# Kernel tuning notes

Measured on AMD Instinct MI355X. Metric: run time of the kernel, lower is better.

The kernel has to match this reference:

```python
import jax, jax.numpy as jnp
import numpy as np

NEG = -9e15

def _gat_layer(x, adj, W, a_src, a_dst):
    # x: [B,N,Fin], W: [Fin,Fout], a_src/a_dst: [Fout], adj: [N,N]
    h = jnp.einsum('bnf,fo->bno', x, W)                    # [B,N,Fout]
    e_src = jnp.einsum('bno,o->bn', h, a_src)              # [B,N]
    e_dst = jnp.einsum('bno,o->bn', h, a_dst)              # [B,N]
    e = jax.nn.leaky_relu(e_src[:, :, None] + e_dst[:, None, :], 0.2)  # [B,N,N]
    att = jax.nn.softmax(jnp.where(adj > 0, e, NEG), axis=-1)
    return jnp.einsum('bij,bjo->bio', att, h)              # [B,N,Fout]

def setup_inputs() -> dict:
    key = jax.random.key(0)
    ks = jax.random.split(key, 12)
    B, N, Fin = 8, 2048, 128
    H = [128, 128, 64]
    C = 128
    s = lambda *d: 1.0 / np.sqrt(d[0])
    inp = {
        'x':   jax.random.normal(ks[0], (B, N, Fin), jnp.float32),
        'adj': jax.random.normal(ks[1], (N, N), jnp.float32),
        'W1':  jax.random.normal(ks[2], (Fin, H[0]), jnp.float32) * s(Fin),
        'a1s': jax.random.normal(ks[3], (H[0],), jnp.float32) * s(H[0]),
        'a1d': jax.random.normal(ks[4], (H[0],), jnp.float32) * s(H[0]),
        'W2':  jax.random.normal(ks[5], (H[0], H[1]), jnp.float32) * s(H[0]),
        'a2s': jax.random.normal(ks[6], (H[1],), jnp.float32) * s(H[1]),
        'a2d': jax.random.normal(ks[7], (H[1],), jnp.float32) * s(H[1]),
        'W3':  jax.random.normal(ks[8], (H[1], H[2]), jnp.float32) * s(H[1]),
        'a3s': jax.random.normal(ks[9], (H[2],), jnp.float32) * s(H[2]),
        'a3d': jax.random.normal(ks[10], (H[2],), jnp.float32) * s(H[2]),
        'Wlin': jax.random.normal(ks[11], (H[2] * N, C), jnp.float32) * s(H[2] * N),
        'blin': jnp.zeros((C,), jnp.float32),
    }
    return inp

def reference(x, adj, W1, a1s, a1d, W2, a2s, a2d, W3, a3s, a3d, Wlin, blin):
    out = jax.nn.relu(_gat_layer(x, adj, W1, a1s, a1d))
    out = jax.nn.relu(_gat_layer(out, adj, W2, a2s, a2d))
    out = jax.nn.relu(_gat_layer(out, adj, W3, a3s, a3d))
    B = out.shape[0]
    out = out.reshape(B, -1)              # flatten [B, N*H3]
    return out @ Wlin + blin              # [B, num_classes]
```

## Files before the change

### kernel.cpp

```cpp
#include <hip/hip_runtime.h>
#include <stdint.h>


typedef unsigned short u16;
typedef __bf16 bf16x8 __attribute__((ext_vector_type(8)));
typedef float f32x4 __attribute__((ext_vector_type(4)));
typedef u16 u16x8 __attribute__((ext_vector_type(8)));

#define LOG2E 1.44269504088896340736f

__device__ __forceinline__ float b2f(u16 u) {
    union { unsigned int i; float f; } v; v.i = ((unsigned int)u) << 16; return v.f;
}
__device__ __forceinline__ u16 f2b(float f) {
    union { float f; unsigned int i; } v; v.f = f;
    unsigned int i = v.i;
    return (u16)((i + 0x7fffu + ((i >> 16) & 1u)) >> 16);
}
__device__ __forceinline__ float fast_exp2(float x) {
#if __has_builtin(__builtin_amdgcn_exp2f)
    return __builtin_amdgcn_exp2f(x);
#else
    return exp2f(x);
#endif
}

union ABfrag { bf16x8 v; u16x8 u; };

__device__ __forceinline__ void gload_lds16(const u16* g, u16* l) {
    __builtin_amdgcn_global_load_lds((const __attribute__((address_space(1))) void*)g,
                                     (__attribute__((address_space(3))) void*)l,
                                     16, 0, 0);
}

__global__ void __launch_bounds__(256) k_mask(const float* __restrict__ adj,
                                              uint32_t* __restrict__ adjm) {
    const int w = threadIdx.x >> 6, lane = threadIdx.x & 63;
    const int row = blockIdx.x * 4 + w;
    const float* ar = adj + (size_t)row * 2048;
    uint32_t* mr = adjm + (size_t)row * 64;
    for (int j0 = 0; j0 < 2048; j0 += 64) {
        unsigned long long m = __ballot(ar[j0 + lane] > 0.f);
        if (lane == 0) {
            mr[(j0 >> 5)] = (uint32_t)m;
            mr[(j0 >> 5) + 1] = (uint32_t)(m >> 32);
        }
    }
}

__global__ void k_prep(const float* __restrict__ W1, const float* __restrict__ W2,
                       const float* __restrict__ W3,
                       const float* __restrict__ a1s, const float* __restrict__ a1d,
                       const float* __restrict__ a2s, const float* __restrict__ a2d,
                       const float* __restrict__ a3s, const float* __restrict__ a3d,
                       u16* __restrict__ Wt1, u16* __restrict__ Wt2, u16* __restrict__ Wt3,
                       float* __restrict__ u1s, float* __restrict__ u1d,
                       float* __restrict__ u2s, float* __restrict__ u2d,
                       float* __restrict__ u3s, float* __restrict__ u3d) {
    if (blockIdx.x == 160) {
        int f = threadIdx.x;
        if (f < 128) {
            float s1 = 0.f, d1 = 0.f, s2 = 0.f, d2 = 0.f, s3 = 0.f, d3 = 0.f;
            for (int o = 0; o < 128; ++o) { float w = W1[f * 128 + o]; s1 += w * a1s[o]; d1 += w * a1d[o]; }
            for (int o = 0; o < 128; ++o) { float w = W2[f * 128 + o]; s2 += w * a2s[o]; d2 += w * a2d[o]; }
            for (int o = 0; o <  64; ++o) { float w = W3[f *  64 + o]; s3 += w * a3s[o]; d3 += w * a3d[o]; }
            u1s[f] = s1 * LOG2E; u1d[f] = d1 * LOG2E;
            u2s[f] = s2 * LOG2E; u2d[f] = d2 * LOG2E;
            u3s[f] = s3 * LOG2E; u3d[f] = d3 * LOG2E;
        }
        return;
    }
    int idx = blockIdx.x * 256 + threadIdx.x;
    if (idx < 16384) {
        int f = idx >> 7, o = idx & 127;
        Wt1[o * 128 + f] = f2b(W1[idx]);
    } else if (idx < 32768) {
        int j = idx - 16384; int f = j >> 7, o = j & 127;
        Wt2[o * 128 + f] = f2b(W2[j]);
    } else if (idx < 40960) {
        int j = idx - 32768; int f = j >> 6, o = j & 63;
        Wt3[o * 128 + f] = f2b(W3[j]);
    }
}

template <int F, bool XF32>
__global__ void __launch_bounds__(256) k_h(const void* __restrict__ xv,
                                           const u16* __restrict__ Wt,
                                           const float* __restrict__ us,
                                           const float* __restrict__ ud,
                                           u16* __restrict__ h_t,
                                           float* __restrict__ es2,
                                           float* __restrict__ ed2) {
    constexpr int NT = F / 16;
    constexpr int TNP = 72;
    __shared__ __align__(16) u16 hl[F * TNP];

    const int b = blockIdx.x;
    const int nblk = blockIdx.y;
    const int tid = threadIdx.x;
    const int w = tid >> 6, lane = tid & 63;
    const int quad = lane >> 4, l15 = lane & 15;
    const int n0w = nblk * 64 + w * 16;
    const int i_a = n0w + l15;

    ABfrag afr[4];
    float ps = 0.f, pd = 0.f;
    if (XF32) {
        const float* xr = (const float*)xv + ((size_t)(b * 2048 + i_a)) * 128;
#pragma unroll
        for (int kk = 0; kk < 4; ++kk) {
            const int o8 = kk * 32 + quad * 8;
            float4 x0 = *reinterpret_cast<const float4*>(xr + o8);
            float4 x1 = *reinterpret_cast<const float4*>(xr + o8 + 4);
            float4 s0 = *reinterpret_cast<const float4*>(us + o8);
            float4 s1 = *reinterpret_cast<const float4*>(us + o8 + 4);
            float4 d0 = *reinterpret_cast<const float4*>(ud + o8);
            float4 d1 = *reinterpret_cast<const float4*>(ud + o8 + 4);
            ps += x0.x * s0.x + x0.y * s0.y + x0.z * s0.z + x0.w * s0.w
                + x1.x * s1.x + x1.y * s1.y + x1.z * s1.z + x1.w * s1.w;
            pd += x0.x * d0.x + x0.y * d0.y + x0.z * d0.z + x0.w * d0.w
                + x1.x * d1.x + x1.y * d1.y + x1.z * d1.z + x1.w * d1.w;
            afr[kk].u[0] = f2b(x0.x); afr[kk].u[1] = f2b(x0.y);
            afr[kk].u[2] = f2b(x0.z); afr[kk].u[3] = f2b(x0.w);
            afr[kk].u[4] = f2b(x1.x); afr[kk].u[5] = f2b(x1.y);
            afr[kk].u[6] = f2b(x1.z); afr[kk].u[7] = f2b(x1.w);
        }
    } else {
        const u16* xr = (const u16*)xv + ((size_t)(b * 2048 + i_a)) * 128;
#pragma unroll
        for (int kk = 0; kk < 4; ++kk) {
            const int o8 = kk * 32 + quad * 8;
            u16x8 xa = *reinterpret_cast<const u16x8*>(xr + o8);
            afr[kk].u = xa;
            float4 s0 = *reinterpret_cast<const float4*>(us + o8);
            float4 s1 = *reinterpret_cast<const float4*>(us + o8 + 4);
            float4 d0 = *reinterpret_cast<const float4*>(ud + o8);
            float4 d1 = *reinterpret_cast<const float4*>(ud + o8 + 4);
            float xf[8];
#pragma unroll
            for (int j = 0; j < 8; ++j) xf[j] = b2f(xa[j]);
            ps += xf[0] * s0.x + xf[1] * s0.y + xf[2] * s0.z + xf[3] * s0.w
                + xf[4] * s1.x + xf[5] * s1.y + xf[6] * s1.z + xf[7] * s1.w;
            pd += xf[0] * d0.x + xf[1] * d0.y + xf[2] * d0.z + xf[3] * d0.w
                + xf[4] * d1.x + xf[5] * d1.y + xf[6] * d1.z + xf[7] * d1.w;
        }
    }
    ps += __shfl_xor(ps, 16, 64); ps += __shfl_xor(ps, 32, 64);
    pd += __shfl_xor(pd, 16, 64); pd += __shfl_xor(pd, 32, 64);
    if (quad == 0) {
        es2[b * 2048 + i_a] = ps;
        ed2[b * 2048 + i_a] = pd;
    }

    f32x4 acc[NT];
#pragma unroll
    for (int nt = 0; nt < NT; ++nt) acc[nt] = (f32x4){0.f, 0.f, 0.f, 0.f};
#pragma unroll
    for (int kk = 0; kk < 4; ++kk) {
#pragma unroll
        for (int nt = 0; nt < NT; ++nt) {
            bf16x8 bfv = *reinterpret_cast<const bf16x8*>(
                Wt + (nt * 16 + l15) * 128 + kk * 32 + quad * 8);
            acc[nt] = __builtin_amdgcn_mfma_f32_16x16x32_bf16(afr[kk].v, bfv, acc[nt], 0, 0, 0);
        }
    }

#pragma unroll
    for (int nt = 0; nt < NT; ++nt)
#pragma unroll
        for (int r = 0; r < 4; ++r)
            hl[(nt * 16 + l15) * TNP + w * 16 + quad * 4 + r] = f2b(acc[nt][r]);
    __syncthreads();
    if (tid < F * 2) {
        int o = tid >> 1, half = tid & 1;
        const u16* src = hl + o * TNP + half * 32;
        u16* dst = h_t + ((size_t)(b * F + o)) * 2048 + nblk * 64 + half * 32;
#pragma unroll
        for (int c = 0; c < 4; ++c)
            *reinterpret_cast<u16x8*>(dst + c * 8) =
                *reinterpret_cast<const u16x8*>(src + c * 8);
    }
}

template <int F, bool OUT_F32>
__global__ void __launch_bounds__(512) k_attn(const float* __restrict__ es2,
                                              const float* __restrict__ ed2,
                                              const uint32_t* __restrict__ adjm,
                                              const u16* __restrict__ h_t,
                                              void* __restrict__ outp) {
    constexpr int NT = F / 16;
    __shared__ __align__(16) u16 Ht[2][2][F * 64];
    __shared__ float dLDS[2][64];
    float* accLDS = (float*)&Ht[0][0][0];

    const int b = blockIdx.x;
    const int iblk = blockIdx.y;
    const int tid = threadIdx.x;
    const int grp = tid >> 8;
    const int t8 = tid & 255;
    const int w = t8 >> 6;
    const int lane = tid & 63;
    const int quad = lane >> 4, l15 = lane & 15;
    const int i_a = iblk * 64 + w * 16 + l15;

    const float esv = es2[b * 2048 + i_a];
    const float* edb = ed2 + b * 2048;
    const uint2* mrow = (const uint2*)(adjm + (size_t)i_a * 64);
    const u16* hb = h_t + (size_t)b * F * 2048;

    const int lro = lane >> 3;
    const int lcp = lane & 7;
    const int jt0 = grp * 16;

    f32x4 acc[NT];
#pragma unroll
    for (int nt = 0; nt < NT; ++nt) acc[nt] = (f32x4){0.f, 0.f, 0.f, 0.f};
    float dacc = 0.f;

    {
        const int j0 = jt0 * 64;
#pragma unroll
        for (int it = 0; it < F / 32; ++it) {
            int ro = (it * 4 + w) * 8 + lro;
            int c = lcp ^ (ro & 7);
            gload_lds16(hb + (size_t)ro * 2048 + j0 + c * 8, &Ht[grp][0][(it * 4 + w) * 512]);
        }
    }
    float4 ec0 = *reinterpret_cast<const float4*>(edb + jt0 * 64 + quad * 8);
    float4 ec1 = *reinterpret_cast<const float4*>(edb + jt0 * 64 + quad * 8 + 4);
    float4 ec2 = *reinterpret_cast<const float4*>(edb + jt0 * 64 + quad * 8 + 32);
    float4 ec3 = *reinterpret_cast<const float4*>(edb + jt0 * 64 + quad * 8 + 36);
    uint2 mc = mrow[jt0];
    __syncthreads();

    for (int jj = 0; jj < 16; ++jj) {
        const int cur = jj & 1, nxt = cur ^ 1;
        float4 en0, en1, en2, en3; uint2 mn;
        if (jj < 15) {
            const int j1 = (jt0 + jj + 1) * 64;
#pragma unroll
            for (int it = 0; it < F / 32; ++it) {
                int ro = (it * 4 + w) * 8 + lro;
                int c = lcp ^ (ro & 7);
                gload_lds16(hb + (size_t)ro * 2048 + j1 + c * 8, &Ht[grp][nxt][(it * 4 + w) * 512]);
            }
            en0 = *reinterpret_cast<const float4*>(edb + j1 + quad * 8);
            en1 = *reinterpret_cast<const float4*>(edb + j1 + quad * 8 + 4);
            en2 = *reinterpret_cast<const float4*>(edb + j1 + quad * 8 + 32);
            en3 = *reinterpret_cast<const float4*>(edb + j1 + quad * 8 + 36);
            mn = mrow[jt0 + jj + 1];
        }

        ABfrag af[2];
        {
            float ed[16] = {ec0.x, ec0.y, ec0.z, ec0.w, ec1.x, ec1.y, ec1.z, ec1.w,
                            ec2.x, ec2.y, ec2.z, ec2.w, ec3.x, ec3.y, ec3.z, ec3.w};
#pragma unroll
            for (int kk = 0; kk < 2; ++kk) {
                uint32_t word = kk ? mc.y : mc.x;
#pragma unroll
                for (int jx = 0; jx < 8; ++jx) {
                    float e = esv + ed[kk * 8 + jx];
                    float v = fmaxf(e, 0.2f * e);
                    float wv = fast_exp2(v);
                    bool bit = (word >> (quad * 8 + jx)) & 1u;
                    wv = bit ? wv : 0.f;
                    u16 wb = f2b(wv);
                    af[kk].u[jx] = wb;
                    dacc += b2f(wb);
                }
            }
        }

#pragma unroll
        for (int kk = 0; kk < 2; ++kk) {
#pragma unroll
            for (int nt = 0; nt < NT; ++nt) {
                int ob = nt * 16 + l15;
                int c = kk * 4 + quad;
                bf16x8 bfv = *reinterpret_cast<const bf16x8*>(
                    &Ht[grp][cur][ob * 64 + ((c ^ (ob & 7)) * 8)]);
                acc[nt] = __builtin_amdgcn_mfma_f32_16x16x32_bf16(af[kk].v, bfv, acc[nt], 0, 0, 0);
            }
        }

        if (jj < 15) { ec0 = en0; ec1 = en1; ec2 = en2; ec3 = en3; mc = mn; }
        __syncthreads();
    }

    dacc += __shfl_xor(dacc, 16, 64);
    dacc += __shfl_xor(dacc, 32, 64);
    if (quad == 0) dLDS[grp][w * 16 + l15] = dacc;
    if (grp == 1) {
#pragma unroll
        for (int nt = 0; nt < NT; ++nt)
            *reinterpret_cast<f32x4*>(&accLDS[(t8 * NT + nt) * 4]) = acc[nt];
    }
    __syncthreads();
    if (grp == 0) {
#pragma unroll
        for (int nt = 0; nt < NT; ++nt)
            acc[nt] += *reinterpret_cast<const f32x4*>(&accLDS[(t8 * NT + nt) * 4]);
        float dinv[4];
#pragma unroll
        for (int r = 0; r < 4; ++r) {
            int row = w * 16 + quad * 4 + r;
            dinv[r] = 1.0f / fmaxf(dLDS[0][row] + dLDS[1][row], 1e-30f);
        }
        const int ib = iblk * 64 + w * 16 + quad * 4;
        if (OUT_F32) {
            float* o3 = (float*)outp;
#pragma unroll
            for (int nt = 0; nt < NT; ++nt)
#pragma unroll
                for (int r = 0; r < 4; ++r) {
                    float vv = fmaxf(acc[nt][r] * dinv[r], 0.f);
                    o3[((size_t)(b * 2048 + ib + r)) * F + nt * 16 + l15] = vv;
                }
        } else {
            u16* xo = (u16*)outp;
#pragma unroll
            for (int nt = 0; nt < NT; ++nt)
#pragma unroll
                for (int r = 0; r < 4; ++r) {
                    float vv = fmaxf(acc[nt][r] * dinv[r], 0.f);
                    xo[((size_t)(b * 2048 + ib + r)) * F + nt * 16 + l15] = f2b(vv);
                }
        }
    }
}

__global__ void __launch_bounds__(256) k_lin(const float* __restrict__ o3,
                                             const float* __restrict__ Wlin,
                                             float* __restrict__ pbuf) {
    __shared__ float xc[8][256];
    __shared__ float red[8][8][128];
    const int tid = threadIdx.x;
    const int k0 = blockIdx.x * 256;
    for (int idx = tid; idx < 2048; idx += 256) {
        int bb = idx >> 8, kk = idx & 255;
        xc[bb][kk] = o3[(size_t)bb * 131072 + k0 + kk];
    }
    __syncthreads();
    const int o4 = tid & 31;
    const int kb = tid >> 5;
    f32x4 acc[8];
#pragma unroll
    for (int bb = 0; bb < 8; ++bb) acc[bb] = (f32x4){0.f, 0.f, 0.f, 0.f};
    const float* wp = Wlin + (size_t)(k0 + kb * 32) * 128 + o4 * 4;
#pragma unroll 4
    for (int k = 0; k < 32; ++k) {
        f32x4 wv = *reinterpret_cast<const f32x4*>(wp + (size_t)k * 128);
#pragma unroll
        for (int bb = 0; bb < 8; ++bb) acc[bb] += wv * xc[bb][kb * 32 + k];
    }
#pragma unroll
    for (int bb = 0; bb < 8; ++bb)
        *reinterpret_cast<f32x4*>(&red[kb][bb][o4 * 4]) = acc[bb];
    __syncthreads();
    const int f = tid * 4;
    const int bb = f >> 7, o = f & 127;
    f32x4 s = (f32x4){0.f, 0.f, 0.f, 0.f};
#pragma unroll
    for (int k2 = 0; k2 < 8; ++k2) s += *reinterpret_cast<const f32x4*>(&red[k2][bb][o]);
    *reinterpret_cast<f32x4*>(&pbuf[(size_t)blockIdx.x * 1024 + f]) = s;
}

__global__ void __launch_bounds__(256) k_bias(const float* __restrict__ pbuf,
                                              const float* __restrict__ blin,
                                              float* __restrict__ out) {
    __shared__ float red[256];
    const int tid = threadIdx.x;
    const int p16 = tid >> 4;
    const int fo = tid & 15;
    const int f0 = blockIdx.x * 16;
    float s = 0.f;
#pragma unroll 4
    for (int p = p16; p < 512; p += 16)
        s += pbuf[(size_t)p * 1024 + f0 + fo];
    red[tid] = s;
    __syncthreads();
    if (tid < 16) {
        float t = 0.f;
#pragma unroll
        for (int k = 0; k < 16; ++k) t += red[k * 16 + tid];
        out[f0 + tid] = t + blin[(f0 + tid) & 127];
    }
}

extern "C" void kernel_launch(void* const* d_in, const int* in_sizes, int n_in,
                              void* d_out, int out_size, void* d_ws, size_t ws_size,
                              hipStream_t stream) {
    (void)in_sizes; (void)n_in; (void)out_size;
    const float* x    = (const float*)d_in[0];
    const float* adj  = (const float*)d_in[1];
    const float* W1   = (const float*)d_in[2];
    const float* a1s  = (const float*)d_in[3];
    const float* a1d  = (const float*)d_in[4];
    const float* W2   = (const float*)d_in[5];
    const float* a2s  = (const float*)d_in[6];
    const float* a2d  = (const float*)d_in[7];
    const float* W3   = (const float*)d_in[8];
    const float* a3s  = (const float*)d_in[9];
    const float* a3d  = (const float*)d_in[10];
    const float* Wlin = (const float*)d_in[11];
    const float* blin = (const float*)d_in[12];

    char* ws = (char*)d_ws;
    u16*   h_t = (u16*)ws;
    size_t off = (size_t)4 << 20;
    float* es2 = (float*)(ws + off); off += 65536;
    float* ed2 = (float*)(ws + off); off += 65536;
    u16*   Wt1 = (u16*)(ws + off);   off += 32768;
    u16*   Wt2 = (u16*)(ws + off);   off += 32768;
    u16*   Wt3 = (u16*)(ws + off);   off += 16384;
    float* u1s = (float*)(ws + off); off += 512;
    float* u1d = (float*)(ws + off); off += 512;
    float* u2s = (float*)(ws + off); off += 512;
    float* u2d = (float*)(ws + off); off += 512;
    float* u3s = (float*)(ws + off); off += 512;
    float* u3d = (float*)(ws + off); off += 512;
    uint32_t* adjm = (uint32_t*)(ws + off); off += 524288;
    float* pbuf = (float*)(ws + off); off += (size_t)512 * 1024 * 4;
    u16* actA;
    if (ws_size >= off + ((size_t)4 << 20)) {
        actA = (u16*)(ws + off);
    } else {
        actA = (u16*)d_in[0];
    }
    float* o3 = (float*)actA;

    dim3 g(8, 32);
    k_mask<<<512, 256, 0, stream>>>(adj, adjm);
    k_prep<<<161, 256, 0, stream>>>(W1, W2, W3, a1s, a1d, a2s, a2d, a3s, a3d,
                                    Wt1, Wt2, Wt3, u1s, u1d, u2s, u2d, u3s, u3d);

    k_h<128, true ><<<g, 256, 0, stream>>>((const void*)x, Wt1, u1s, u1d, h_t, es2, ed2);
    k_attn<128, false><<<g, 512, 0, stream>>>(es2, ed2, adjm, h_t, (void*)actA);

    k_h<128, false><<<g, 256, 0, stream>>>((const void*)actA, Wt2, u2s, u2d, h_t, es2, ed2);
    k_attn<128, false><<<g, 512, 0, stream>>>(es2, ed2, adjm, h_t, (void*)actA);

    k_h<64, false><<<g, 256, 0, stream>>>((const void*)actA, Wt3, u3s, u3d, h_t, es2, ed2);
    k_attn<64, true ><<<g, 512, 0, stream>>>(es2, ed2, adjm, h_t, (void*)o3);

    k_lin<<<512, 256, 0, stream>>>(o3, Wlin, pbuf);
    k_bias<<<64, 256, 0, stream>>>(pbuf, blin, (float*)d_out);
}
```

Before: 260.1 us.

## Factor exp of leaky-relu logits into per-node exponentials and MFMA row sums

Precomputes exp2 of source and destination scores (and of their 0.2-scaled versions) per node in the projection kernel. The attention kernel then forms each weight as the max of two products, with no per-edge exp. The softmax denominator is accumulated by an extra MFMA against a ones fragment instead of scalar adds and shuffles. This removes per-edge transcendental and VALU work, at the cost of doubled score storage and a possible overflow or precision change from the product form.

Result: no change. 264.6 us (+1.7%).

```diff
diff --git a/kernel.cpp b/kernel.cpp
--- a/kernel.cpp
+++ b/kernel.cpp
@@ -89,8 +89,8 @@
                                            const float* __restrict__ us,
                                            const float* __restrict__ ud,
                                            u16* __restrict__ h_t,
-                                           float* __restrict__ es2,
-                                           float* __restrict__ ed2) {
+                                           float* __restrict__ esf,
+                                           float* __restrict__ edf) {
     constexpr int NT = F / 16;
     constexpr int TNP = 72;
     __shared__ __align__(16) u16 hl[F * TNP];
@@ -148,8 +148,11 @@
     ps += __shfl_xor(ps, 16, 64); ps += __shfl_xor(ps, 32, 64);
     pd += __shfl_xor(pd, 16, 64); pd += __shfl_xor(pd, 32, 64);
     if (quad == 0) {
-        es2[b * 2048 + i_a] = ps;
-        ed2[b * 2048 + i_a] = pd;
+        const size_t idx = (size_t)(b * 2048 + i_a) * 2;
+        float2 sv; sv.x = fast_exp2(ps); sv.y = fast_exp2(0.2f * ps);
+        float2 dv; dv.x = fast_exp2(pd); dv.y = fast_exp2(0.2f * pd);
+        *reinterpret_cast<float2*>(esf + idx) = sv;
+        *reinterpret_cast<float2*>(edf + idx) = dv;
     }
 
     f32x4 acc[NT];
@@ -183,14 +186,13 @@
 }
 
 template <int F, bool OUT_F32>
-__global__ void __launch_bounds__(512) k_attn(const float* __restrict__ es2,
-                                              const float* __restrict__ ed2,
+__global__ void __launch_bounds__(512) k_attn(const float* __restrict__ esf,
+                                              const float* __restrict__ edf,
                                               const uint32_t* __restrict__ adjm,
                                               const u16* __restrict__ h_t,
                                               void* __restrict__ outp) {
     constexpr int NT = F / 16;
     __shared__ __align__(16) u16 Ht[2][2][F * 64];
-    __shared__ float dLDS[2][64];
     float* accLDS = (float*)&Ht[0][0][0];
 
     const int b = blockIdx.x;
@@ -203,8 +205,9 @@
     const int quad = lane >> 4, l15 = lane & 15;
     const int i_a = iblk * 64 + w * 16 + l15;
 
-    const float esv = es2[b * 2048 + i_a];
-    const float* edb = ed2 + b * 2048;
+    const float2 esp = *reinterpret_cast<const float2*>(esf + ((size_t)(b * 2048 + i_a)) * 2);
+    const float Es = esp.x, Fs = esp.y;
+    const float* edb = edf + (size_t)b * 4096;
     const uint2* mrow = (const uint2*)(adjm + (size_t)i_a * 64);
     const u16* hb = h_t + (size_t)b * F * 2048;
 
@@ -212,10 +215,14 @@
     const int lcp = lane & 7;
     const int jt0 = grp * 16;
 
+    ABfrag onesf;
+#pragma unroll
+    for (int j = 0; j < 8; ++j) onesf.u[j] = 0x3F80;
+
     f32x4 acc[NT];
 #pragma unroll
     for (int nt = 0; nt < NT; ++nt) acc[nt] = (f32x4){0.f, 0.f, 0.f, 0.f};
-    float dacc = 0.f;
+    f32x4 dccc = (f32x4){0.f, 0.f, 0.f, 0.f};
 
     {
         const int j0 = jt0 * 64;
@@ -226,16 +233,21 @@
             gload_lds16(hb + (size_t)ro * 2048 + j0 + c * 8, &Ht[grp][0][(it * 4 + w) * 512]);
         }
     }
-    float4 ec0 = *reinterpret_cast<const float4*>(edb + jt0 * 64 + quad * 8);
-    float4 ec1 = *reinterpret_cast<const float4*>(edb + jt0 * 64 + quad * 8 + 4);
-    float4 ec2 = *reinterpret_cast<const float4*>(edb + jt0 * 64 + quad * 8 + 32);
-    float4 ec3 = *reinterpret_cast<const float4*>(edb + jt0 * 64 + quad * 8 + 36);
+    f32x4 ec[8];
+    {
+        const float* eb = edb + (size_t)(jt0 * 64 + quad * 8) * 2;
+#pragma unroll
+        for (int q = 0; q < 4; ++q) ec[q] = *reinterpret_cast<const f32x4*>(eb + q * 4);
+#pragma unroll
+        for (int q = 0; q < 4; ++q) ec[4 + q] = *reinterpret_cast<const f32x4*>(eb + 64 + q * 4);
+    }
     uint2 mc = mrow[jt0];
     __syncthreads();
 
+#pragma unroll 2
     for (int jj = 0; jj < 16; ++jj) {
         const int cur = jj & 1, nxt = cur ^ 1;
-        float4 en0, en1, en2, en3; uint2 mn;
+        f32x4 en[8]; uint2 mn;
         if (jj < 15) {
             const int j1 = (jt0 + jj + 1) * 64;
 #pragma unroll
@@ -244,31 +256,29 @@
                 int c = lcp ^ (ro & 7);
                 gload_lds16(hb + (size_t)ro * 2048 + j1 + c * 8, &Ht[grp][nxt][(it * 4 + w) * 512]);
             }
-            en0 = *reinterpret_cast<const float4*>(edb + j1 + quad * 8);
-            en1 = *reinterpret_cast<const float4*>(edb + j1 + quad * 8 + 4);
-            en2 = *reinterpret_cast<const float4*>(edb + j1 + quad * 8 + 32);
-            en3 = *reinterpret_cast<const float4*>(edb + j1 + quad * 8 + 36);
+            const float* eb = edb + (size_t)(j1 + quad * 8) * 2;
+#pragma unroll
+            for (int q = 0; q < 4; ++q) en[q] = *reinterpret_cast<const f32x4*>(eb + q * 4);
+#pragma unroll
+            for (int q = 0; q < 4; ++q) en[4 + q] = *reinterpret_cast<const f32x4*>(eb + 64 + q * 4);
             mn = mrow[jt0 + jj + 1];
         }
 
         ABfrag af[2];
-        {
-            float ed[16] = {ec0.x, ec0.y, ec0.z, ec0.w, ec1.x, ec1.y, ec1.z, ec1.w,
-                            ec2.x, ec2.y, ec2.z, ec2.w, ec3.x, ec3.y, ec3.z, ec3.w};
-#pragma unroll
-            for (int kk = 0; kk < 2; ++kk) {
-                uint32_t word = kk ? mc.y : mc.x;
-#pragma unroll
-                for (int jx = 0; jx < 8; ++jx) {
-                    float e = esv + ed[kk * 8 + jx];
-                    float v = fmaxf(e, 0.2f * e);
-                    float wv = fast_exp2(v);
-                    bool bit = (word >> (quad * 8 + jx)) & 1u;
-                    wv = bit ? wv : 0.f;
-                    u16 wb = f2b(wv);
-                    af[kk].u[jx] = wb;
-                    dacc += b2f(wb);
-                }
+#pragma unroll
+        for (int kk = 0; kk < 2; ++kk) {
+            const uint32_t word = kk ? mc.y : mc.x;
+#pragma unroll
+            for (int px = 0; px < 4; ++px) {
+                const f32x4 q = ec[kk * 4 + px];
+                float w0 = fmaxf(Es * q.x, Fs * q.y);
+                float w1 = fmaxf(Es * q.z, Fs * q.w);
+                const uint32_t s0 = 0u - ((word >> (quad * 8 + px * 2)) & 1u);
+                const uint32_t s1 = 0u - ((word >> (quad * 8 + px * 2 + 1)) & 1u);
+                w0 = __uint_as_float(__float_as_uint(w0) & s0);
+                w1 = __uint_as_float(__float_as_uint(w1) & s1);
+                af[kk].v[px * 2]     = (__bf16)w0;
+                af[kk].v[px * 2 + 1] = (__bf16)w1;
             }
         }
 
@@ -282,31 +292,33 @@
                     &Ht[grp][cur][ob * 64 + ((c ^ (ob & 7)) * 8)]);
                 acc[nt] = __builtin_amdgcn_mfma_f32_16x16x32_bf16(af[kk].v, bfv, acc[nt], 0, 0, 0);
             }
-        }
-
-        if (jj < 15) { ec0 = en0; ec1 = en1; ec2 = en2; ec3 = en3; mc = mn; }
+            dccc = __builtin_amdgcn_mfma_f32_16x16x32_bf16(af[kk].v, onesf.v, dccc, 0, 0, 0);
+        }
+
+        if (jj < 15) {
+#pragma unroll
+            for (int q = 0; q < 8; ++q) ec[q] = en[q];
+            mc = mn;
+        }
         __syncthreads();
     }
 
-    dacc += __shfl_xor(dacc, 16, 64);
-    dacc += __shfl_xor(dacc, 32, 64);
-    if (quad == 0) dLDS[grp][w * 16 + l15] = dacc;
     if (grp == 1) {
 #pragma unroll
         for (int nt = 0; nt < NT; ++nt)
-            *reinterpret_cast<f32x4*>(&accLDS[(t8 * NT + nt) * 4]) = acc[nt];
+            *reinterpret_cast<f32x4*>(&accLDS[(t8 * (NT + 1) + nt) * 4]) = acc[nt];
+        *reinterpret_cast<f32x4*>(&accLDS[(t8 * (NT + 1) + NT) * 4]) = dccc;
     }
     __syncthreads();
     if (grp == 0) {
 #pragma unroll
         for (int nt = 0; nt < NT; ++nt)
-            acc[nt] += *reinterpret_cast<const f32x4*>(&accLDS[(t8 * NT + nt) * 4]);
+            acc[nt] += *reinterpret_cast<const f32x4*>(&accLDS[(t8 * (NT + 1) + nt) * 4]);
+        dccc += *reinterpret_cast<const f32x4*>(&accLDS[(t8 * (NT + 1) + NT) * 4]);
         float dinv[4];
 #pragma unroll
-        for (int r = 0; r < 4; ++r) {
-            int row = w * 16 + quad * 4 + r;
-            dinv[r] = 1.0f / fmaxf(dLDS[0][row] + dLDS[1][row], 1e-30f);
-        }
+        for (int r = 0; r < 4; ++r)
+            dinv[r] = 1.0f / fmaxf(dccc[r], 1e-30f);
         const int ib = iblk * 64 + w * 16 + quad * 4;
         if (OUT_F32) {
             float* o3 = (float*)outp;
@@ -409,8 +421,8 @@
     char* ws = (char*)d_ws;
     u16*   h_t = (u16*)ws;
     size_t off = (size_t)4 << 20;
-    float* es2 = (float*)(ws + off); off += 65536;
-    float* ed2 = (float*)(ws + off); off += 65536;
+    float* esf = (float*)(ws + off); off += 131072;
+    float* edf = (float*)(ws + off); off += 131072;
     u16*   Wt1 = (u16*)(ws + off);   off += 32768;
     u16*   Wt2 = (u16*)(ws + off);   off += 32768;
     u16*   Wt3 = (u16*)(ws + off);   off += 16384;
@@ -435,14 +447,14 @@
     k_prep<<<161, 256, 0, stream>>>(W1, W2, W3, a1s, a1d, a2s, a2d, a3s, a3d,
                                     Wt1, Wt2, Wt3, u1s, u1d, u2s, u2d, u3s, u3d);
 
-    k_h<128, true ><<<g, 256, 0, stream>>>((const void*)x, Wt1, u1s, u1d, h_t, es2, ed2);
-    k_attn<128, false><<<g, 512, 0, stream>>>(es2, ed2, adjm, h_t, (void*)actA);
-
-    k_h<128, false><<<g, 256, 0, stream>>>((const void*)actA, Wt2, u2s, u2d, h_t, es2, ed2);
-    k_attn<128, false><<<g, 512, 0, stream>>>(es2, ed2, adjm, h_t, (void*)actA);
-
-    k_h<64, false><<<g, 256, 0, stream>>>((const void*)actA, Wt3, u3s, u3d, h_t, es2, ed2);
-    k_attn<64, true ><<<g, 512, 0, stream>>>(es2, ed2, adjm, h_t, (void*)o3);
+    k_h<128, true ><<<g, 256, 0, stream>>>((const void*)x, Wt1, u1s, u1d, h_t, esf, edf);
+    k_attn<128, false><<<g, 512, 0, stream>>>(esf, edf, adjm, h_t, (void*)actA);
+
+    k_h<128, false><<<g, 256, 0, stream>>>((const void*)actA, Wt2, u2s, u2d, h_t, esf, edf);
+    k_attn<128, false><<<g, 512, 0, stream>>>(esf, edf, adjm, h_t, (void*)actA);
+
+    k_h<64, false><<<g, 256, 0, stream>>>((const void*)actA, Wt3, u3s, u3d, h_t, esf, edf);
+    k_attn<64, true ><<<g, 512, 0, stream>>>(esf, edf, adjm, h_t, (void*)o3);
 
     k_lin<<<512, 256, 0, stream>>>(o3, Wlin, pbuf);
     k_bias<<<64, 256, 0, stream>>>(pbuf, blin, (float*)d_out);
```
